# Kernel tuning notes

Measured on AMD Instinct MI355X. Metric: run time of the kernel, lower is better.

## Reference

```python
import jax, jax.numpy as jnp
import numpy as np

B, C_ENT, C_REL = 32768, 1000, 500


def setup_inputs() -> dict:
    key = jax.random.key(0)
    ks = jax.random.split(key, 6)
    return {
        "sub_input": jax.random.normal(ks[0], (B, C_ENT), dtype=jnp.float32),
        "relation_input": jax.random.normal(ks[1], (B, C_REL), dtype=jnp.float32),
        "obj_input": jax.random.normal(ks[2], (B, C_ENT), dtype=jnp.float32),
        "sub_target": jax.random.randint(ks[3], (B,), 0, C_ENT, dtype=jnp.int32),
        "relation_target": jax.random.randint(ks[4], (B,), 0, C_REL, dtype=jnp.int32),
        "obj_target": jax.random.randint(ks[5], (B,), 0, C_ENT, dtype=jnp.int32),
    }


def reference(sub_input, relation_input, obj_input, sub_target, relation_target, obj_target):
    s = jax.nn.softmax(sub_input, axis=1)
    r = jax.nn.softmax(relation_input, axis=1)
    o = jax.nn.softmax(obj_input, axis=1)
    b = s.shape[0]
    rows = jnp.arange(b)

    # ground-truth triplet probability
    gt = s[rows, sub_target] * r[rows, relation_target] * o[rows, obj_target]

    # top-2 values/indices per row (replaces full torch.sort)
    sv, si = jax.lax.top_k(s, 2)
    rv, ri = jax.lax.top_k(r, 2)
    ov, oi = jax.lax.top_k(o, 2)

    # all three argmaxes match the targets?
    cond = (si[:, 0] == sub_target) & (ri[:, 0] == relation_target) & (oi[:, 0] == obj_target)

    # 8 combinations of top-2 probs; second-smallest of the 8 (torch.sort ascending, index 1)
    tmp = (sv[:, :, None, None] * rv[:, None, :, None] * ov[:, None, None, :]).reshape(b, 8)
    second_smallest = jnp.sort(tmp, axis=1)[:, 1]

    top1 = sv[:, 0] * rv[:, 0] * ov[:, 0]
    pre = jnp.where(cond, second_smallest, top1)

    out = 1.0 - gt + pre
    return jnp.mean(jnp.maximum(out, 0.0))
```

## Files before the change

### kernel.cpp

```cpp
#include <hip/hip_runtime.h>
#include <float.h>
#include <limits.h>


constexpr int B      = 32768;
constexpr int C_ENT  = 1000;
constexpr int C_REL  = 500;


template<int NK, int C4>
__device__ inline float4 wave_stats(const float* __restrict__ row, int lane, int target) {
  const float4* row4 = (const float4*)row;
  float4 v[NK];
#pragma unroll
  for (int k = 0; k < NK; ++k) {
    int i = lane + 64 * k;
    v[k] = (i < C4) ? row4[i] : make_float4(-FLT_MAX, -FLT_MAX, -FLT_MAX, -FLT_MAX);
  }
  float xt = row[target];

  float lm = -FLT_MAX;
#pragma unroll
  for (int k = 0; k < NK; ++k)
    lm = fmaxf(lm, fmaxf(fmaxf(v[k].x, v[k].y), fmaxf(v[k].z, v[k].w)));
#pragma unroll
  for (int off = 32; off; off >>= 1)
    lm = fmaxf(lm, __shfl_xor(lm, off));
  const float m1 = lm;

  float z[NK];
  float m2 = -FLT_MAX;
  int   idx = INT_MAX;
  int   cnt = 0;
#pragma unroll
  for (int k = 0; k < NK; ++k) {
    const int base = 4 * (lane + 64 * k);
    const float a0 = v[k].x, a1 = v[k].y, a2 = v[k].z, a3 = v[k].w;
    z[k] = (__expf(a0 - m1) + __expf(a1 - m1)) + (__expf(a2 - m1) + __expf(a3 - m1));
    const bool e0 = (a0 == m1), e1 = (a1 == m1), e2 = (a2 == m1), e3 = (a3 == m1);
    cnt += (int)e0 + (int)e1 + (int)e2 + (int)e3;
    m2 = fmaxf(m2, fmaxf(e0 ? -FLT_MAX : a0, e1 ? -FLT_MAX : a1));
    m2 = fmaxf(m2, fmaxf(e2 ? -FLT_MAX : a2, e3 ? -FLT_MAX : a3));
    const int i01 = min(e0 ? base     : INT_MAX, e1 ? base + 1 : INT_MAX);
    const int i23 = min(e2 ? base + 2 : INT_MAX, e3 ? base + 3 : INT_MAX);
    idx = min(idx, min(i01, i23));
  }
  float Z;
  if constexpr (NK == 4) Z = (z[0] + z[1]) + (z[2] + z[3]);
  else                   Z = z[0] + z[1];

#pragma unroll
  for (int off = 32; off; off >>= 1) {
    Z   += __shfl_xor(Z, off);
    m2   = fmaxf(m2, __shfl_xor(m2, off));
    cnt += __shfl_xor(cnt, off);
    idx  = min(idx, __shfl_xor(idx, off));
  }
  if (cnt >= 2) m2 = m1;

  const float invZ = 1.0f / Z;
  return make_float4(invZ,
                     __expf(m2 - m1) * invZ,
                     __expf(xt - m1) * invZ,
                     __int_as_float(idx));
}

__global__ __launch_bounds__(256) void stats_kernel(
    const float* __restrict__ s, const float* __restrict__ r, const float* __restrict__ o,
    const int* __restrict__ st, const int* __restrict__ rt, const int* __restrict__ ot,
    float4* __restrict__ out4) {
  const int wid  = threadIdx.x >> 6;
  const int lane = threadIdx.x & 63;
  const int gw   = blockIdx.x * 4 + wid;
  const int m    = gw >> 15;
  const int row  = gw & (B - 1);
  float4 res;
  if (m == 0)      res = wave_stats<4, C_ENT / 4>(s + (size_t)row * C_ENT, lane, st[row]);
  else if (m == 1) res = wave_stats<4, C_ENT / 4>(o + (size_t)row * C_ENT, lane, ot[row]);
  else             res = wave_stats<2, C_REL / 4>(r + (size_t)row * C_REL, lane, rt[row]);
  if (lane == 0) out4[m * B + row] = res;
}

__global__ __launch_bounds__(256) void combine_kernel(
    const float4* __restrict__ stat4,
    const int* __restrict__ st, const int* __restrict__ rt, const int* __restrict__ ot,
    float* __restrict__ partial) {
  const int row = blockIdx.x * 256 + threadIdx.x;
  const float4 S = stat4[row];
  const float4 O = stat4[B + row];
  const float4 R = stat4[2 * B + row];
  const float gt   = S.z * R.z * O.z;
  const float top1 = S.x * R.x * O.x;
  const float c1 = S.x * R.y * O.y;
  const float c2 = S.y * R.x * O.y;
  const float c3 = S.y * R.y * O.x;
  const float second = fminf(c1, fminf(c2, c3));
  const bool cond = (__float_as_int(S.w) == st[row]) &&
                    (__float_as_int(R.w) == rt[row]) &&
                    (__float_as_int(O.w) == ot[row]);
  const float pre = cond ? second : top1;
  partial[row] = fmaxf(1.0f - gt + pre, 0.0f);
}


__device__ inline void combine_stats(float& m1, int& i1, float& m2, float& Z,
                                     float bm1, int bi1, float bm2, float bZ) {
  bool bwin = (bm1 > m1) || (bm1 == m1 && bi1 < i1);
  float wm1 = bwin ? bm1 : m1;
  int   wi1 = bwin ? bi1 : i1;
  float wm2 = bwin ? bm2 : m2;
  float lm1 = bwin ? m1  : bm1;
  float wZ  = bwin ? bZ  : Z;
  float lZ  = bwin ? Z   : bZ;
  m1 = wm1; i1 = wi1;
  m2 = fmaxf(wm2, lm1);
  Z  = wZ + lZ * __expf(lm1 - wm1);
}

template<int NK, int C4>
__device__ inline void row_stats(const float* __restrict__ row, int lane, int target,
                                 float& p_top1, float& p_top2, int& amax, float& p_tgt) {
  const float4* row4 = (const float4*)row;
  float4 v[NK];
#pragma unroll
  for (int k = 0; k < NK; ++k) {
    int idx = lane + 64 * k;
    v[k] = (idx < C4) ? row4[idx] : make_float4(-FLT_MAX, -FLT_MAX, -FLT_MAX, -FLT_MAX);
  }
  float m1 = -FLT_MAX, m2 = -FLT_MAX;
  int   i1 = 0x7fffffff;
#pragma unroll
  for (int k = 0; k < NK; ++k) {
    int base = 4 * (lane + 64 * k);
    float a0 = v[k].x, a1 = v[k].y, a2 = v[k].z, a3 = v[k].w;
    if (a0 > m1) { m2 = m1; m1 = a0; i1 = base;     } else if (a0 > m2) m2 = a0;
    if (a1 > m1) { m2 = m1; m1 = a1; i1 = base + 1; } else if (a1 > m2) m2 = a1;
    if (a2 > m1) { m2 = m1; m1 = a2; i1 = base + 2; } else if (a2 > m2) m2 = a2;
    if (a3 > m1) { m2 = m1; m1 = a3; i1 = base + 3; } else if (a3 > m2) m2 = a3;
  }
  float Z = 0.f;
#pragma unroll
  for (int k = 0; k < NK; ++k) {
    Z += __expf(v[k].x - m1); Z += __expf(v[k].y - m1);
    Z += __expf(v[k].z - m1); Z += __expf(v[k].w - m1);
  }
#pragma unroll
  for (int off = 32; off > 0; off >>= 1) {
    float bm1 = __shfl_xor(m1, off);
    int   bi1 = __shfl_xor(i1, off);
    float bm2 = __shfl_xor(m2, off);
    float bZ  = __shfl_xor(Z,  off);
    combine_stats(m1, i1, m2, Z, bm1, bi1, bm2, bZ);
  }
  float invZ = 1.0f / Z;
  float xt   = row[target];
  p_top1 = invZ;
  p_top2 = __expf(m2 - m1) * invZ;
  p_tgt  = __expf(xt - m1) * invZ;
  amax   = i1;
}

template<bool ATOMIC>
__global__ __launch_bounds__(256) void rank_loss_kernel(
    const float* __restrict__ s, const float* __restrict__ r, const float* __restrict__ o,
    const int* __restrict__ st, const int* __restrict__ rt, const int* __restrict__ ot,
    float* __restrict__ partial, float* __restrict__ out) {
  const int wid  = threadIdx.x >> 6;
  const int lane = threadIdx.x & 63;
  const int row  = blockIdx.x * 4 + wid;

  const float* srow = s + (size_t)row * C_ENT;
  const float* rrow = r + (size_t)row * C_REL;
  const float* orow = o + (size_t)row * C_ENT;
  const int tS = st[row], tR = rt[row], tO = ot[row];

  float sp0, sp1, spt; int sa;
  float rp0, rp1, rpt; int ra;
  float op0, op1, opt; int oa;
  row_stats<4, C_ENT / 4>(srow, lane, tS, sp0, sp1, sa, spt);
  row_stats<2, C_REL / 4>(rrow, lane, tR, rp0, rp1, ra, rpt);
  row_stats<4, C_ENT / 4>(orow, lane, tO, op0, op1, oa, opt);

  if (lane == 0) {
    float gt   = spt * rpt * opt;
    float top1 = sp0 * rp0 * op0;
    float c1 = sp0 * rp1 * op1;
    float c2 = sp1 * rp0 * op1;
    float c3 = sp1 * rp1 * op0;
    float second = fminf(c1, fminf(c2, c3));
    bool cond = (sa == tS) && (ra == tR) && (oa == tO);
    float pre = cond ? second : top1;
    float val = fmaxf(1.0f - gt + pre, 0.0f);
    if (ATOMIC) atomicAdd(out, val * (1.0f / (float)B));
    else        partial[row] = val;
  }
}


__global__ __launch_bounds__(1024) void reduce_sum_kernel(const float* __restrict__ p,
                                                          float* __restrict__ out) {
  const float4* p4 = (const float4*)p;
  float sum = 0.f;
  for (int i = threadIdx.x; i < B / 4; i += 1024) {
    float4 v = p4[i];
    sum += (v.x + v.y) + (v.z + v.w);
  }
#pragma unroll
  for (int off = 32; off > 0; off >>= 1) sum += __shfl_xor(sum, off);
  __shared__ float lds[16];
  if ((threadIdx.x & 63) == 0) lds[threadIdx.x >> 6] = sum;
  __syncthreads();
  if (threadIdx.x == 0) {
    float t = 0.f;
#pragma unroll
    for (int i = 0; i < 16; ++i) t += lds[i];
    out[0] = t * (1.0f / (float)B);
  }
}

extern "C" void kernel_launch(void* const* d_in, const int* in_sizes, int n_in,
                              void* d_out, int out_size, void* d_ws, size_t ws_size,
                              hipStream_t stream) {
  const float* s  = (const float*)d_in[0];
  const float* r  = (const float*)d_in[1];
  const float* o  = (const float*)d_in[2];
  const int*   st = (const int*)d_in[3];
  const int*   rt = (const int*)d_in[4];
  const int*   ot = (const int*)d_in[5];
  float* out = (float*)d_out;

  const size_t statBytes = (size_t)3 * B * sizeof(float4);
  if (ws_size >= statBytes + (size_t)B * sizeof(float)) {
    float4* stat4  = (float4*)d_ws;
    float* partial = (float*)((char*)d_ws + statBytes);
    stats_kernel<<<3 * B / 4, 256, 0, stream>>>(s, r, o, st, rt, ot, stat4);
    combine_kernel<<<B / 256, 256, 0, stream>>>(stat4, st, rt, ot, partial);
    reduce_sum_kernel<<<1, 1024, 0, stream>>>(partial, out);
  } else if (ws_size >= (size_t)B * sizeof(float)) {
    float* partial = (float*)d_ws;
    rank_loss_kernel<false><<<B / 4, 256, 0, stream>>>(s, r, o, st, rt, ot, partial, nullptr);
    reduce_sum_kernel<<<1, 1024, 0, stream>>>(partial, out);
  } else {
    hipMemsetAsync(d_out, 0, sizeof(float), stream);
    rank_loss_kernel<true><<<B / 4, 256, 0, stream>>>(s, r, o, st, rt, ot, nullptr, out);
  }
}
```

Baseline: 322.3 us.

## Process two rows per wavefront with top-2 max tracking in stats kernel

Each wavefront now handles two rows of the same matrix instead of one, interleaving their loads and shuffle reductions to raise memory-level parallelism and halve the wave count. The max and second-max are computed together in a single pass with a per-lane top-2 tournament and a merged shuffle reduction, which replaces the separate max reduction plus the equality-count logic. The tail load is clamped rather than predicated. Register pressure per wave rises, which may reduce occupancy.

```diff
diff --git a/kernel.cpp b/kernel.cpp
--- a/kernel.cpp
+++ b/kernel.cpp
@@ -8,77 +8,131 @@
 constexpr int C_REL  = 500;
 
 
-template<int NK, int C4>
-__device__ inline float4 wave_stats(const float* __restrict__ row, int lane, int target) {
-  const float4* row4 = (const float4*)row;
-  float4 v[NK];
-#pragma unroll
-  for (int k = 0; k < NK; ++k) {
-    int i = lane + 64 * k;
-    v[k] = (i < C4) ? row4[i] : make_float4(-FLT_MAX, -FLT_MAX, -FLT_MAX, -FLT_MAX);
-  }
-  float xt = row[target];
-
-  float lm = -FLT_MAX;
-#pragma unroll
-  for (int k = 0; k < NK; ++k)
-    lm = fmaxf(lm, fmaxf(fmaxf(v[k].x, v[k].y), fmaxf(v[k].z, v[k].w)));
-#pragma unroll
-  for (int off = 32; off; off >>= 1)
-    lm = fmaxf(lm, __shfl_xor(lm, off));
-  const float m1 = lm;
-
-  float z[NK];
-  float m2 = -FLT_MAX;
-  int   idx = INT_MAX;
-  int   cnt = 0;
+template<int NK>
+__device__ inline void lane_top2(const float4* v, float& m1, float& m2) {
+  float hi[2 * NK], lo[2 * NK];
+#pragma unroll
+  for (int k = 0; k < NK; ++k) {
+    hi[2 * k]     = fmaxf(v[k].x, v[k].y);
+    lo[2 * k]     = fminf(v[k].x, v[k].y);
+    hi[2 * k + 1] = fmaxf(v[k].z, v[k].w);
+    lo[2 * k + 1] = fminf(v[k].z, v[k].w);
+  }
+#pragma unroll
+  for (int half = NK; half >= 1; half >>= 1) {
+#pragma unroll
+    for (int i = 0; i < half; ++i) {
+      const float ha = hi[i], hb = hi[i + half];
+      const float la = lo[i], lb = lo[i + half];
+      hi[i] = fmaxf(ha, hb);
+      lo[i] = fmaxf(fmaxf(la, lb), fminf(ha, hb));
+    }
+  }
+  m1 = hi[0];
+  m2 = lo[0];
+}
+
+template<int NK>
+__device__ inline void lane_z_idx(const float4* v, int lane, float m1, float& z, int& idx) {
+  float zp[NK];
+  idx = INT_MAX;
 #pragma unroll
   for (int k = 0; k < NK; ++k) {
     const int base = 4 * (lane + 64 * k);
     const float a0 = v[k].x, a1 = v[k].y, a2 = v[k].z, a3 = v[k].w;
-    z[k] = (__expf(a0 - m1) + __expf(a1 - m1)) + (__expf(a2 - m1) + __expf(a3 - m1));
-    const bool e0 = (a0 == m1), e1 = (a1 == m1), e2 = (a2 == m1), e3 = (a3 == m1);
-    cnt += (int)e0 + (int)e1 + (int)e2 + (int)e3;
-    m2 = fmaxf(m2, fmaxf(e0 ? -FLT_MAX : a0, e1 ? -FLT_MAX : a1));
-    m2 = fmaxf(m2, fmaxf(e2 ? -FLT_MAX : a2, e3 ? -FLT_MAX : a3));
-    const int i01 = min(e0 ? base     : INT_MAX, e1 ? base + 1 : INT_MAX);
-    const int i23 = min(e2 ? base + 2 : INT_MAX, e3 ? base + 3 : INT_MAX);
+    zp[k] = (__expf(a0 - m1) + __expf(a1 - m1)) + (__expf(a2 - m1) + __expf(a3 - m1));
+    const int i01 = min(a0 == m1 ? base     : INT_MAX, a1 == m1 ? base + 1 : INT_MAX);
+    const int i23 = min(a2 == m1 ? base + 2 : INT_MAX, a3 == m1 ? base + 3 : INT_MAX);
     idx = min(idx, min(i01, i23));
   }
-  float Z;
-  if constexpr (NK == 4) Z = (z[0] + z[1]) + (z[2] + z[3]);
-  else                   Z = z[0] + z[1];
+  if constexpr (NK == 4) z = (zp[0] + zp[1]) + (zp[2] + zp[3]);
+  else                   z = zp[0] + zp[1];
+}
+
+template<int NK, int C4>
+__device__ inline void wave_stats2(const float* __restrict__ rowA,
+                                   const float* __restrict__ rowB,
+                                   int lane, int tA, int tB,
+                                   float4* __restrict__ outp) {
+  const float4* a4 = (const float4*)rowA;
+  const float4* b4 = (const float4*)rowB;
+  float4 va[NK], vb[NK];
+#pragma unroll
+  for (int k = 0; k < NK - 1; ++k) {
+    va[k] = a4[lane + 64 * k];
+    vb[k] = b4[lane + 64 * k];
+  }
+  {
+    const int  i  = lane + 64 * (NK - 1);
+    const bool ok = (i < C4);
+    const int  ic = ok ? i : (C4 - 1);
+    float4 ta = a4[ic], tb = b4[ic];
+    ta.x = ok ? ta.x : -FLT_MAX;  ta.y = ok ? ta.y : -FLT_MAX;
+    ta.z = ok ? ta.z : -FLT_MAX;  ta.w = ok ? ta.w : -FLT_MAX;
+    tb.x = ok ? tb.x : -FLT_MAX;  tb.y = ok ? tb.y : -FLT_MAX;
+    tb.z = ok ? tb.z : -FLT_MAX;  tb.w = ok ? tb.w : -FLT_MAX;
+    va[NK - 1] = ta;
+    vb[NK - 1] = tb;
+  }
+  const float xa = rowA[tA];
+  const float xb = rowB[tB];
+
+  float m1a, m2a, m1b, m2b;
+  lane_top2<NK>(va, m1a, m2a);
+  lane_top2<NK>(vb, m1b, m2b);
 
 #pragma unroll
   for (int off = 32; off; off >>= 1) {
-    Z   += __shfl_xor(Z, off);
-    m2   = fmaxf(m2, __shfl_xor(m2, off));
-    cnt += __shfl_xor(cnt, off);
-    idx  = min(idx, __shfl_xor(idx, off));
-  }
-  if (cnt >= 2) m2 = m1;
-
-  const float invZ = 1.0f / Z;
-  return make_float4(invZ,
-                     __expf(m2 - m1) * invZ,
-                     __expf(xt - m1) * invZ,
-                     __int_as_float(idx));
-}
-
-__global__ __launch_bounds__(256) void stats_kernel(
+    const float p1a = __shfl_xor(m1a, off), p2a = __shfl_xor(m2a, off);
+    const float p1b = __shfl_xor(m1b, off), p2b = __shfl_xor(m2b, off);
+    m2a = fmaxf(fmaxf(m2a, p2a), fminf(m1a, p1a));
+    m1a = fmaxf(m1a, p1a);
+    m2b = fmaxf(fmaxf(m2b, p2b), fminf(m1b, p1b));
+    m1b = fmaxf(m1b, p1b);
+  }
+
+  float za, zb;
+  int   ia, ib;
+  lane_z_idx<NK>(va, lane, m1a, za, ia);
+  lane_z_idx<NK>(vb, lane, m1b, zb, ib);
+
+#pragma unroll
+  for (int off = 32; off; off >>= 1) {
+    za += __shfl_xor(za, off);
+    zb += __shfl_xor(zb, off);
+    ia  = min(ia, __shfl_xor(ia, off));
+    ib  = min(ib, __shfl_xor(ib, off));
+  }
+
+  if (lane == 0) {
+    const float iZa = 1.0f / za;
+    const float iZb = 1.0f / zb;
+    outp[0] = make_float4(iZa, __expf(m2a - m1a) * iZa, __expf(xa - m1a) * iZa,
+                          __int_as_float(ia));
+    outp[1] = make_float4(iZb, __expf(m2b - m1b) * iZb, __expf(xb - m1b) * iZb,
+                          __int_as_float(ib));
+  }
+}
+
+__global__ __launch_bounds__(256) void stats2_kernel(
     const float* __restrict__ s, const float* __restrict__ r, const float* __restrict__ o,
     const int* __restrict__ st, const int* __restrict__ rt, const int* __restrict__ ot,
     float4* __restrict__ out4) {
   const int wid  = threadIdx.x >> 6;
   const int lane = threadIdx.x & 63;
   const int gw   = blockIdx.x * 4 + wid;
-  const int m    = gw >> 15;
-  const int row  = gw & (B - 1);
-  float4 res;
-  if (m == 0)      res = wave_stats<4, C_ENT / 4>(s + (size_t)row * C_ENT, lane, st[row]);
-  else if (m == 1) res = wave_stats<4, C_ENT / 4>(o + (size_t)row * C_ENT, lane, ot[row]);
-  else             res = wave_stats<2, C_REL / 4>(r + (size_t)row * C_REL, lane, rt[row]);
-  if (lane == 0) out4[m * B + row] = res;
+  const int m    = gw >> 14;
+  const int p    = gw & 16383;
+  const int row  = 2 * p;
+  if (m == 0)
+    wave_stats2<4, C_ENT / 4>(s + (size_t)row * C_ENT, s + (size_t)(row + 1) * C_ENT,
+                              lane, st[row], st[row + 1], out4 + row);
+  else if (m == 1)
+    wave_stats2<4, C_ENT / 4>(o + (size_t)row * C_ENT, o + (size_t)(row + 1) * C_ENT,
+                              lane, ot[row], ot[row + 1], out4 + B + row);
+  else
+    wave_stats2<2, C_REL / 4>(r + (size_t)row * C_REL, r + (size_t)(row + 1) * C_REL,
+                              lane, rt[row], rt[row + 1], out4 + 2 * B + row);
 }
 
 __global__ __launch_bounds__(256) void combine_kernel(
@@ -233,7 +287,7 @@
   if (ws_size >= statBytes + (size_t)B * sizeof(float)) {
     float4* stat4  = (float4*)d_ws;
     float* partial = (float*)((char*)d_ws + statBytes);
-    stats_kernel<<<3 * B / 4, 256, 0, stream>>>(s, r, o, st, rt, ot, stat4);
+    stats2_kernel<<<3 * B / 8, 256, 0, stream>>>(s, r, o, st, rt, ot, stat4);
     combine_kernel<<<B / 256, 256, 0, stream>>>(stat4, st, rt, ot, partial);
     reduce_sum_kernel<<<1, 1024, 0, stream>>>(partial, out);
   } else if (ws_size >= (size_t)B * sizeof(float)) {
```

Result: no change. 320.1 us (-0.7%).
